# Kernel optimization log

Hardware: AMD Instinct MI355X
Metric: run time of the kernel (lower is better)

Reference implementation:

```python
import jax, jax.numpy as jnp
import numpy as np

B, S, D, H = 2, 2048, 2048, 16
HD = D // H  # 128


def setup_inputs() -> dict:
    key = jax.random.key(0)
    ks = jax.random.split(key, 5)
    scale = 0.02
    return {
        "hidden_states": jax.random.normal(ks[0], (B, S, D), dtype=jnp.float32),
        "Wqkv_w": jax.random.normal(ks[1], (3 * D, D), dtype=jnp.float32) * scale,
        "Wqkv_b": jax.random.normal(ks[2], (3 * D,), dtype=jnp.float32) * scale,
        "out_w": jax.random.normal(ks[3], (D, D), dtype=jnp.float32) * scale,
        "out_b": jax.random.normal(ks[4], (D,), dtype=jnp.float32) * scale,
    }


def reference(hidden_states, Wqkv_w, Wqkv_b, out_w, out_b):
    b, s, d = hidden_states.shape
    # QKV projection (torch Linear: x @ W.T + b)
    qkv = hidden_states @ Wqkv_w.T + Wqkv_b          # [b, s, 3d]
    qkv = qkv.reshape(b, s, 3, H, HD)                 # 'b s (three h d)'
    q, k, v = qkv[:, :, 0], qkv[:, :, 1], qkv[:, :, 2]  # [b, s, h, hd]
    softmax_scale = 1.0 / np.float32(np.sqrt(HD))
    # full quadratic scores, matching the naive baddbmm path
    scores = jnp.einsum('bthd,bshd->bhts', q, k) * softmax_scale  # [b,h,t,s]
    # causal=False (module default), dropout_p=0.0 -> no mask, no dropout
    attn = jax.nn.softmax(scores, axis=-1)
    ctx = jnp.einsum('bhts,bshd->bthd', attn, v)      # [b, t, h, hd]
    ctx = ctx.reshape(b, s, d)
    return ctx @ out_w.T + out_b
```

## Files before the change

### kernel.cpp

```cpp
#include <hip/hip_runtime.h>
#include <cstdint>
#include <cstddef>

#define B_ 2
#define S_ 2048
#define D_ 2048
#define H_ 16
#define HD_ 128
#define NTOK 4096
#define NQKV 6144

typedef unsigned short u16;
typedef __attribute__((ext_vector_type(8))) __bf16 bf16x8;
typedef __attribute__((ext_vector_type(4))) float f32x4;

__device__ __forceinline__ u16 f2bf(float f) {
  uint32_t u = __builtin_bit_cast(uint32_t, f);
  u = (u + 0x7FFFu + ((u >> 16) & 1u)) >> 16;
  return (u16)u;
}

__device__ __forceinline__ void gload_lds16(const void* g, void* l) {
  __builtin_amdgcn_global_load_lds(
      (const __attribute__((address_space(1))) void*)g,
      (__attribute__((address_space(3))) void*)l, 16, 0, 0);
}

__global__ void cvt_all(const float* __restrict__ hs, const float* __restrict__ wqkv,
                        const float* __restrict__ wo,
                        u16* __restrict__ hsb, u16* __restrict__ wqkvb,
                        u16* __restrict__ wob) {
  const int n1 = (B_ * S_ * D_) / 8;
  const int n2 = n1 + (NQKV * D_) / 8;
  const int n3 = n2 + (D_ * D_) / 8;
  int idx = blockIdx.x * blockDim.x + threadIdx.x;
  int stride = gridDim.x * blockDim.x;
  for (int i = idx; i < n3; i += stride) {
    const float* src; u16* dst; int j;
    if (i < n1)      { src = hs;   dst = hsb;   j = i; }
    else if (i < n2) { src = wqkv; dst = wqkvb; j = i - n1; }
    else             { src = wo;   dst = wob;   j = i - n2; }
    const float4* s = (const float4*)(src + (size_t)j * 8);
    float4 a = s[0], b = s[1];
    union { u16 u[8]; uint4 v; } o;
    o.u[0] = f2bf(a.x); o.u[1] = f2bf(a.y); o.u[2] = f2bf(a.z); o.u[3] = f2bf(a.w);
    o.u[4] = f2bf(b.x); o.u[5] = f2bf(b.y); o.u[6] = f2bf(b.z); o.u[7] = f2bf(b.w);
    *(uint4*)(dst + (size_t)j * 8) = o.v;
  }
}

#define PH_MID() do { asm volatile("s_barrier" ::: "memory"); \
  __builtin_amdgcn_s_setprio(1); } while (0)
#define PH_END() do { __builtin_amdgcn_s_setprio(0); \
  asm volatile("s_barrier" ::: "memory"); } while (0)
#define PH_END_VM(n) do { __builtin_amdgcn_s_setprio(0); \
  asm volatile("s_waitcnt vmcnt(" #n ")" ::: "memory"); \
  asm volatile("s_barrier" ::: "memory"); } while (0)


#define STA(sl,buf,ko) gload_lds16(aSrc + (size_t)(sl)*64*D_ + (ko), aDst + (buf)*8192  + (sl)*4096)
#define STB(sl,buf,ko) gload_lds16(bSrc + (size_t)(sl)*64*D_ + (ko), bDst + (buf)*12288 + (sl)*4096)

#define LOADB(buf) do { _Pragma("unroll") for (int nf = 0; nf < 3; ++nf) \
  _Pragma("unroll") for (int kk = 0; kk < 2; ++kk) \
    breg[nf][kk] = *(const bf16x8*)(sB + (buf)*12288 + (wn*48 + nf*16 + fr)*64 + ((((kk<<2)|fq)^swz)<<3)); } while (0)
#define LOADA_A(buf,q) do { _Pragma("unroll") for (int mm = 0; mm < 2; ++mm) \
  _Pragma("unroll") for (int kk = 0; kk < 2; ++kk) \
    arA[mm][kk] = *(const bf16x8*)(sA + (buf)*8192 + (wm*64 + ((q)*2+mm)*16 + fr)*64 + ((((kk<<2)|fq)^swz)<<3)); } while (0)
#define LOADA_B(buf,q) do { _Pragma("unroll") for (int mm = 0; mm < 2; ++mm) \
  _Pragma("unroll") for (int kk = 0; kk < 2; ++kk) \
    arB[mm][kk] = *(const bf16x8*)(sA + (buf)*8192 + (wm*64 + ((q)*2+mm)*16 + fr)*64 + ((((kk<<2)|fq)^swz)<<3)); } while (0)
#define MFMA12_A(q) do { _Pragma("unroll") for (int kk = 0; kk < 2; ++kk) \
  _Pragma("unroll") for (int mm = 0; mm < 2; ++mm) \
  _Pragma("unroll") for (int nf = 0; nf < 3; ++nf) \
    acc[(q)*2+mm][nf] = __builtin_amdgcn_mfma_f32_16x16x32_bf16(arA[mm][kk], breg[nf][kk], acc[(q)*2+mm][nf], 0, 0, 0); } while (0)
#define MFMA12_B(q) do { _Pragma("unroll") for (int kk = 0; kk < 2; ++kk) \
  _Pragma("unroll") for (int mm = 0; mm < 2; ++mm) \
  _Pragma("unroll") for (int nf = 0; nf < 3; ++nf) \
    acc[(q)*2+mm][nf] = __builtin_amdgcn_mfma_f32_16x16x32_bf16(arB[mm][kk], breg[nf][kk], acc[(q)*2+mm][nf], 0, 0, 0); } while (0)

__global__ __launch_bounds__(512, 4) void qkv_gemm(
    const u16* __restrict__ hsb, const u16* __restrict__ wb,
    const float* __restrict__ bias,
    u16* __restrict__ qb, u16* __restrict__ kb, u16* __restrict__ vT)
{
  __shared__ alignas(1024) u16 sA[2 * 8192];
  __shared__ alignas(1024) u16 sB[2 * 12288];
  const int tid = threadIdx.x;
  const int lane = tid & 63, wid = tid >> 6;
  const int wm = wid >> 2, wn = wid & 3;
  const int fr = lane & 15, fq = lane >> 4;
  const int swz = fr & 7;
  const int m0 = blockIdx.x * 128, n0 = blockIdx.y * 192;

  const int r8 = tid >> 3, g8 = (tid & 7) ^ (r8 & 7);
  const u16* aSrc = hsb + (size_t)(m0 + r8) * D_ + g8 * 8;
  const u16* bSrc = wb  + (size_t)(n0 + r8) * D_ + g8 * 8;
  u16* aDst = sA + wid * 512;
  u16* bDst = sB + wid * 512;

  f32x4 acc[4][3];
  f32x4 z = {0.f, 0.f, 0.f, 0.f};
#pragma unroll
  for (int m = 0; m < 4; ++m)
#pragma unroll
    for (int n = 0; n < 3; ++n) acc[m][n] = z;

  bf16x8 breg[3][2], arA[2][2], arB[2][2];

  STB(0,0,0); STB(1,0,0); STB(2,0,0); STA(0,0,0); STA(1,0,0);
  STB(0,1,64); STB(1,1,64); STB(2,1,64);
  asm volatile("s_waitcnt vmcnt(3)" ::: "memory");
  asm volatile("s_barrier" ::: "memory");

#pragma unroll 1
  for (int j = 0; j < 15; ++j) {
    const int kA1 = (2*j + 1) * 64;
    const int kB2 = (2*j + 2) * 64;
    const int kB3 = (2*j + 3) * 64;
    LOADB(0); LOADA_A(0,0); LOADA_B(0,1); STA(0,1,kA1); STA(1,1,kA1);
      PH_MID(); MFMA12_A(0); PH_END();
    STB(0,0,kB2); STB(1,0,kB2); STB(2,0,kB2);
      PH_MID(); MFMA12_B(1); PH_END_VM(3);
    LOADB(1); LOADA_A(1,0); LOADA_B(1,1); STA(0,0,kB2); STA(1,0,kB2);
      PH_MID(); MFMA12_A(0); PH_END();
    STB(0,1,kB3); STB(1,1,kB3); STB(2,1,kB3);
      PH_MID(); MFMA12_B(1); PH_END_VM(3);
  }
  {
    const int kA31 = 31 * 64;
    LOADB(0); LOADA_A(0,0); LOADA_B(0,1); STA(0,1,kA31); STA(1,1,kA31);
      PH_MID(); MFMA12_A(0); PH_END();
      PH_MID(); MFMA12_B(1); PH_END_VM(0);
    LOADB(1); LOADA_A(1,0); LOADA_B(1,1);
      PH_MID(); MFMA12_A(0); PH_END();
      PH_MID(); MFMA12_B(1); PH_END();
  }

  const float qscale = 0.08838834764831845f;
#pragma unroll
  for (int mf = 0; mf < 4; ++mf)
#pragma unroll
    for (int nf = 0; nf < 3; ++nf) {
      int col = n0 + wn * 48 + nf * 16 + fr;
      float bv = bias[col];
      int t = col >> 11;
      int d2 = col & 2047;
      int h = d2 >> 7, hd = d2 & 127;
#pragma unroll
      for (int r = 0; r < 4; ++r) {
        int row = m0 + wm * 64 + mf * 16 + fq * 4 + r;
        int bb = row >> 11, s = row & 2047;
        int bh = bb * H_ + h;
        float val = acc[mf][nf][r] + bv;
        if (t == 0)      qb[((size_t)bh * S_ + s) * HD_ + hd] = f2bf(val * qscale);
        else if (t == 1) kb[((size_t)bh * S_ + s) * HD_ + hd] = f2bf(val);
        else             vT[((size_t)bh * HD_ + hd) * S_ + s] = f2bf(val);
      }
    }
}

#define OSTA(sl,buf,ko) gload_lds16(aSrcO + (size_t)(sl)*64*D_ + (ko), aDstO + (buf)*8192 + (sl)*4096)
#define OSTB(sl,buf,ko) gload_lds16(bSrcO + (size_t)(sl)*64*D_ + (ko), bDstO + (buf)*8192 + (sl)*4096)

#define OLOADB(buf) do { _Pragma("unroll") for (int nf = 0; nf < 2; ++nf) \
  _Pragma("unroll") for (int kk = 0; kk < 2; ++kk) \
    obreg[nf][kk] = *(const bf16x8*)(sB + (buf)*8192 + (wn*32 + nf*16 + fr)*64 + ((((kk<<2)|fq)^swz)<<3)); } while (0)
#define OLOADA_A(buf,q) do { _Pragma("unroll") for (int mm = 0; mm < 2; ++mm) \
  _Pragma("unroll") for (int kk = 0; kk < 2; ++kk) \
    oarA[mm][kk] = *(const bf16x8*)(sA + (buf)*8192 + (wm*64 + ((q)*2+mm)*16 + fr)*64 + ((((kk<<2)|fq)^swz)<<3)); } while (0)
#define OLOADA_B(buf,q) do { _Pragma("unroll") for (int mm = 0; mm < 2; ++mm) \
  _Pragma("unroll") for (int kk = 0; kk < 2; ++kk) \
    oarB[mm][kk] = *(const bf16x8*)(sA + (buf)*8192 + (wm*64 + ((q)*2+mm)*16 + fr)*64 + ((((kk<<2)|fq)^swz)<<3)); } while (0)
#define OMFMA8_A(q) do { _Pragma("unroll") for (int kk = 0; kk < 2; ++kk) \
  _Pragma("unroll") for (int mm = 0; mm < 2; ++mm) \
  _Pragma("unroll") for (int nf = 0; nf < 2; ++nf) \
    acc[(q)*2+mm][nf] = __builtin_amdgcn_mfma_f32_16x16x32_bf16(oarA[mm][kk], obreg[nf][kk], acc[(q)*2+mm][nf], 0, 0, 0); } while (0)
#define OMFMA8_B(q) do { _Pragma("unroll") for (int kk = 0; kk < 2; ++kk) \
  _Pragma("unroll") for (int mm = 0; mm < 2; ++mm) \
  _Pragma("unroll") for (int nf = 0; nf < 2; ++nf) \
    acc[(q)*2+mm][nf] = __builtin_amdgcn_mfma_f32_16x16x32_bf16(oarB[mm][kk], obreg[nf][kk], acc[(q)*2+mm][nf], 0, 0, 0); } while (0)

__global__ __launch_bounds__(512, 4) void out_gemm(
    const u16* __restrict__ ctx, const u16* __restrict__ wo,
    const float* __restrict__ bias, float* __restrict__ out)
{
  __shared__ alignas(1024) u16 sA[2 * 8192];
  __shared__ alignas(1024) u16 sB[2 * 8192];
  const int tid = threadIdx.x;
  const int lane = tid & 63, wid = tid >> 6;
  const int wm = wid >> 2, wn = wid & 3;
  const int fr = lane & 15, fq = lane >> 4;
  const int swz = fr & 7;
  const int m0 = blockIdx.x * 128, n0 = blockIdx.y * 128;

  const int r8 = tid >> 3, g8 = (tid & 7) ^ (r8 & 7);
  const u16* aSrcO = ctx + (size_t)(m0 + r8) * D_ + g8 * 8;
  const u16* bSrcO = wo  + (size_t)(n0 + r8) * D_ + g8 * 8;
  u16* aDstO = sA + wid * 512;
  u16* bDstO = sB + wid * 512;

  f32x4 acc[4][2];
  f32x4 z = {0.f, 0.f, 0.f, 0.f};
#pragma unroll
  for (int m = 0; m < 4; ++m)
#pragma unroll
    for (int n = 0; n < 2; ++n) acc[m][n] = z;

  bf16x8 obreg[2][2], oarA[2][2], oarB[2][2];

  OSTB(0,0,0); OSTB(1,0,0); OSTA(0,0,0); OSTA(1,0,0);
  OSTB(0,1,64); OSTB(1,1,64);
  asm volatile("s_waitcnt vmcnt(2)" ::: "memory");
  asm volatile("s_barrier" ::: "memory");

#pragma unroll 1
  for (int j = 0; j < 15; ++j) {
    const int kA1 = (2*j + 1) * 64;
    const int kB2 = (2*j + 2) * 64;
    const int kB3 = (2*j + 3) * 64;
    OLOADB(0); OLOADA_A(0,0); OLOADA_B(0,1); OSTA(0,1,kA1); OSTA(1,1,kA1);
      PH_MID(); OMFMA8_A(0); PH_END();
    OSTB(0,0,kB2); OSTB(1,0,kB2);
      PH_MID(); OMFMA8_B(1); PH_END_VM(2);
    OLOADB(1); OLOADA_A(1,0); OLOADA_B(1,1); OSTA(0,0,kB2); OSTA(1,0,kB2);
      PH_MID(); OMFMA8_A(0); PH_END();
    OSTB(0,1,kB3); OSTB(1,1,kB3);
      PH_MID(); OMFMA8_B(1); PH_END_VM(2);
  }
  {
    const int kA31 = 31 * 64;
    OLOADB(0); OLOADA_A(0,0); OLOADA_B(0,1); OSTA(0,1,kA31); OSTA(1,1,kA31);
      PH_MID(); OMFMA8_A(0); PH_END();
      PH_MID(); OMFMA8_B(1); PH_END_VM(0);
    OLOADB(1); OLOADA_A(1,0); OLOADA_B(1,1);
      PH_MID(); OMFMA8_A(0); PH_END();
      PH_MID(); OMFMA8_B(1); PH_END();
  }

#pragma unroll
  for (int mf = 0; mf < 4; ++mf)
#pragma unroll
    for (int nf = 0; nf < 2; ++nf) {
      int col = n0 + wn * 32 + nf * 16 + fr;
      float bv = bias[col];
#pragma unroll
      for (int r = 0; r < 4; ++r) {
        int row = m0 + wm * 64 + mf * 16 + fq * 4 + r;
        out[(size_t)row * D_ + col] = acc[mf][nf][r] + bv;
      }
    }
}

#define STAGEKV(kvv, buf) do { _Pragma("unroll") \
  for (int i = 0; i < 4; ++i) { \
    int lk = i * 256 + tid; int rk = lk >> 4, sk = lk & 15; \
    gload_lds16(Kg + (size_t)((kvv) + rk) * HD_ + ((sk ^ (rk & 7)) << 3), \
                &Kl[buf][i * 2048 + wid * 512]); \
    int rv = lk >> 3, sv = lk & 7; \
    gload_lds16(Vg + (size_t)rv * S_ + (kvv) + ((sv ^ (rv & 7)) << 3), \
                &Vl[buf][i * 2048 + wid * 512]); \
  } } while (0)

__global__ __launch_bounds__(256, 2) void attn(
    const u16* __restrict__ qb, const u16* __restrict__ kb,
    const u16* __restrict__ vT, u16* __restrict__ ctx)
{
  __shared__ alignas(1024) u16 Kl[2][64 * 128];
  __shared__ alignas(1024) u16 Vl[2][128 * 64];
  __shared__ alignas(16) u16 Pl[4][32 * 64];

  const int tid = threadIdx.x, lane = tid & 63, wid = tid >> 6;
  const int fr = lane & 15, fq = lane >> 4;
  const int bh = blockIdx.y;
  const int q0 = blockIdx.x * 128 + wid * 32;
  f32x4 z = {0.f, 0.f, 0.f, 0.f};

  const u16* Kg = kb + (size_t)bh * S_ * HD_;
  const u16* Vg = vT + (size_t)bh * HD_ * S_;

  STAGEKV(0, 0);

  const u16* qbase = qb + ((size_t)bh * S_ + q0) * HD_;
  bf16x8 qa[2][4];
#pragma unroll
  for (int h = 0; h < 2; ++h)
#pragma unroll
    for (int kc = 0; kc < 4; ++kc)
      qa[h][kc] = *(const bf16x8*)(qbase + (size_t)(h * 16 + fr) * HD_ + kc * 32 + fq * 8);

  f32x4 accv[2][8];
#pragma unroll
  for (int h = 0; h < 2; ++h)
#pragma unroll
    for (int n = 0; n < 8; ++n) accv[h][n] = z;
  float m_run[2] = {-1e30f, -1e30f};
  float l_run[2] = {0.f, 0.f};

  __syncthreads();
  int cur = 0;

  for (int kv = 0; kv < S_; kv += 64) {
    if (kv + 64 < S_) STAGEKV(kv + 64, cur ^ 1);

    const u16* Kc = Kl[cur];
    const u16* Vc = Vl[cur];

    f32x4 sc[2][4];
    __builtin_amdgcn_s_setprio(1);
#pragma unroll
    for (int j = 0; j < 4; ++j) {
      f32x4 s0 = z, s1 = z;
#pragma unroll
      for (int kc = 0; kc < 4; ++kc) {
        int row = j * 16 + fr;
        bf16x8 kf = *(const bf16x8*)&Kc[row * 128 + ((kc * 32 + fq * 8) ^ ((row & 7) << 3))];
        s0 = __builtin_amdgcn_mfma_f32_16x16x32_bf16(kf, qa[0][kc], s0, 0, 0, 0);
        s1 = __builtin_amdgcn_mfma_f32_16x16x32_bf16(kf, qa[1][kc], s1, 0, 0, 0);
      }
      sc[0][j] = s0; sc[1][j] = s1;
    }
    __builtin_amdgcn_s_setprio(0);

    float pmax[2];
#pragma unroll
    for (int h = 0; h < 2; ++h) {
      float mx = sc[h][0][0];
#pragma unroll
      for (int j = 0; j < 4; ++j)
#pragma unroll
        for (int r = 0; r < 4; ++r) mx = fmaxf(mx, sc[h][j][r]);
      mx = fmaxf(mx, __shfl_xor(mx, 16));
      mx = fmaxf(mx, __shfl_xor(mx, 32));
      pmax[h] = mx;
    }

    int need = (pmax[0] > m_run[0] + 8.f) || (pmax[1] > m_run[1] + 8.f);
    if (__any(need)) {
#pragma unroll
      for (int h = 0; h < 2; ++h) {
        float mn = fmaxf(m_run[h], pmax[h]);
        float corr = __expf(m_run[h] - mn);
        m_run[h] = mn;
        l_run[h] *= corr;
#pragma unroll
        for (int r = 0; r < 4; ++r) {
          float rc = __shfl(corr, (lane & 48) | (fq * 4 + r));
#pragma unroll
          for (int n = 0; n < 8; ++n) accv[h][n][r] *= rc;
        }
      }
    }

    u16* Pw = Pl[wid];
#pragma unroll
    for (int h = 0; h < 2; ++h) {
      float ls = 0.f;
#pragma unroll
      for (int j = 0; j < 4; ++j) {
        union { u16 u[4]; ushort4 v; } pk;
#pragma unroll
        for (int r = 0; r < 4; ++r) {
          float p = __expf(sc[h][j][r] - m_run[h]);
          ls += p;
          pk.u[r] = f2bf(p);
        }
        int prow = h * 16 + fr;
        *(ushort4*)&Pw[prow * 64 + ((j * 16 + fq * 4) ^ ((fr & 7) << 3))] = pk.v;
      }
      ls += __shfl_xor(ls, 16);
      ls += __shfl_xor(ls, 32);
      l_run[h] += ls;
    }

    __builtin_amdgcn_s_setprio(1);
#pragma unroll
    for (int kc = 0; kc < 2; ++kc) {
      int pcol = (kc * 32 + fq * 8) ^ ((fr & 7) << 3);
      bf16x8 pa0 = *(const bf16x8*)&Pw[fr * 64 + pcol];
      bf16x8 pa1 = *(const bf16x8*)&Pw[(16 + fr) * 64 + pcol];
#pragma unroll
      for (int n = 0; n < 8; ++n) {
        int row = n * 16 + fr;
        bf16x8 vf = *(const bf16x8*)&Vc[row * 64 + ((kc * 32 + fq * 8) ^ ((row & 7) << 3))];
        accv[0][n] = __builtin_amdgcn_mfma_f32_16x16x32_bf16(pa0, vf, accv[0][n], 0, 0, 0);
        accv[1][n] = __builtin_amdgcn_mfma_f32_16x16x32_bf16(pa1, vf, accv[1][n], 0, 0, 0);
      }
    }
    __builtin_amdgcn_s_setprio(0);

    __syncthreads();
    cur ^= 1;
  }

  float inv[2][4];
#pragma unroll
  for (int h = 0; h < 2; ++h)
#pragma unroll
    for (int r = 0; r < 4; ++r) {
      float l = __shfl(l_run[h], (lane & 48) | (fq * 4 + r));
      inv[h][r] = 1.f / l;
    }
  u16* cb = ctx + (((size_t)(bh >> 4)) * S_ + q0) * D_ + (size_t)(bh & 15) * HD_;
#pragma unroll
  for (int h = 0; h < 2; ++h)
#pragma unroll
    for (int n = 0; n < 8; ++n)
#pragma unroll
      for (int r = 0; r < 4; ++r) {
        int q = h * 16 + fq * 4 + r;
        cb[(size_t)q * D_ + n * 16 + fr] = f2bf(accv[h][n][r] * inv[h][r]);
      }
}

extern "C" void kernel_launch(void* const* d_in, const int* in_sizes, int n_in,
                              void* d_out, int out_size, void* d_ws, size_t ws_size,
                              hipStream_t stream) {
  const float* hs   = (const float*)d_in[0];
  const float* wqkv = (const float*)d_in[1];
  const float* bqkv = (const float*)d_in[2];
  const float* wo   = (const float*)d_in[3];
  const float* bo   = (const float*)d_in[4];
  float* out = (float*)d_out;

  char* ws = (char*)d_ws;
  u16* hsb   = (u16*)(ws);
  u16* wqkvb = (u16*)(ws + 16777216);
  u16* wob   = (u16*)(ws + 41943040);
  u16* qb    = (u16*)(ws + 50331648);
  u16* kb    = (u16*)(ws + 67108864);
  u16* vT    = (u16*)(ws + 83886080);
  u16* ctx   = (u16*)(ws + 100663296);

  cvt_all<<<2048, 256, 0, stream>>>(hs, wqkv, wo, hsb, wqkvb, wob);

  qkv_gemm<<<dim3(NTOK / 128, NQKV / 192), 512, 0, stream>>>(hsb, wqkvb, bqkv, qb, kb, vT);
  attn<<<dim3(S_ / 128, B_ * H_), 256, 0, stream>>>(qb, kb, vT, ctx);
  out_gemm<<<dim3(NTOK / 128, D_ / 128), 512, 0, stream>>>(ctx, wob, bo, out);
}
```

Measured before the change: 285.7 us.

## Load QKV weight tiles directly from global into registers, bypassing LDS

The QKV GEMM stops staging the weight (B) operand through shared memory. Each wave now prefetches its B fragments straight from global memory into double-buffered registers one k-step ahead, while A is still staged through LDS. This removes the B LDS traffic and halves shared memory per block, which may raise occupancy. The cost is uncoalesced-ish 16-byte global loads per lane, duplicated across the two wm waves, and higher register pressure from the two B fragment sets.

Result: slower. 398.5 us (+39.5%).

```diff
diff --git a/kernel.cpp b/kernel.cpp
--- a/kernel.cpp
+++ b/kernel.cpp
@@ -58,26 +58,18 @@
   asm volatile("s_barrier" ::: "memory"); } while (0)
 
 
-#define STA(sl,buf,ko) gload_lds16(aSrc + (size_t)(sl)*64*D_ + (ko), aDst + (buf)*8192  + (sl)*4096)
-#define STB(sl,buf,ko) gload_lds16(bSrc + (size_t)(sl)*64*D_ + (ko), bDst + (buf)*12288 + (sl)*4096)
-
-#define LOADB(buf) do { _Pragma("unroll") for (int nf = 0; nf < 3; ++nf) \
+#define STA(sl,buf,ko) gload_lds16(aSrc + (size_t)(sl)*64*D_ + (ko), aDst + (buf)*8192 + (sl)*4096)
+
+#define LDA(buf,q) do { _Pragma("unroll") for (int mm = 0; mm < 2; ++mm) \
   _Pragma("unroll") for (int kk = 0; kk < 2; ++kk) \
-    breg[nf][kk] = *(const bf16x8*)(sB + (buf)*12288 + (wn*48 + nf*16 + fr)*64 + ((((kk<<2)|fq)^swz)<<3)); } while (0)
-#define LOADA_A(buf,q) do { _Pragma("unroll") for (int mm = 0; mm < 2; ++mm) \
+    ar[mm][kk] = *(const bf16x8*)(sA + (buf)*8192 + (wm*64 + ((q)*2+mm)*16 + fr)*64 + ((((kk<<2)|fq)^swz)<<3)); } while (0)
+#define PREFB(bg, ko) do { _Pragma("unroll") for (int nf = 0; nf < 3; ++nf) \
   _Pragma("unroll") for (int kk = 0; kk < 2; ++kk) \
-    arA[mm][kk] = *(const bf16x8*)(sA + (buf)*8192 + (wm*64 + ((q)*2+mm)*16 + fr)*64 + ((((kk<<2)|fq)^swz)<<3)); } while (0)
-#define LOADA_B(buf,q) do { _Pragma("unroll") for (int mm = 0; mm < 2; ++mm) \
-  _Pragma("unroll") for (int kk = 0; kk < 2; ++kk) \
-    arB[mm][kk] = *(const bf16x8*)(sA + (buf)*8192 + (wm*64 + ((q)*2+mm)*16 + fr)*64 + ((((kk<<2)|fq)^swz)<<3)); } while (0)
-#define MFMA12_A(q) do { _Pragma("unroll") for (int kk = 0; kk < 2; ++kk) \
+    bg[nf][kk] = *(const bf16x8*)(bBase + (size_t)nf * 16 * D_ + (ko) + kk * 32); } while (0)
+#define MFMA12G(bg, base) do { _Pragma("unroll") for (int kk = 0; kk < 2; ++kk) \
   _Pragma("unroll") for (int mm = 0; mm < 2; ++mm) \
   _Pragma("unroll") for (int nf = 0; nf < 3; ++nf) \
-    acc[(q)*2+mm][nf] = __builtin_amdgcn_mfma_f32_16x16x32_bf16(arA[mm][kk], breg[nf][kk], acc[(q)*2+mm][nf], 0, 0, 0); } while (0)
-#define MFMA12_B(q) do { _Pragma("unroll") for (int kk = 0; kk < 2; ++kk) \
-  _Pragma("unroll") for (int mm = 0; mm < 2; ++mm) \
-  _Pragma("unroll") for (int nf = 0; nf < 3; ++nf) \
-    acc[(q)*2+mm][nf] = __builtin_amdgcn_mfma_f32_16x16x32_bf16(arB[mm][kk], breg[nf][kk], acc[(q)*2+mm][nf], 0, 0, 0); } while (0)
+    acc[(base)+mm][nf] = __builtin_amdgcn_mfma_f32_16x16x32_bf16(ar[mm][kk], bg[nf][kk], acc[(base)+mm][nf], 0, 0, 0); } while (0)
 
 __global__ __launch_bounds__(512, 4) void qkv_gemm(
     const u16* __restrict__ hsb, const u16* __restrict__ wb,
@@ -85,7 +77,6 @@
     u16* __restrict__ qb, u16* __restrict__ kb, u16* __restrict__ vT)
 {
   __shared__ alignas(1024) u16 sA[2 * 8192];
-  __shared__ alignas(1024) u16 sB[2 * 12288];
   const int tid = threadIdx.x;
   const int lane = tid & 63, wid = tid >> 6;
   const int wm = wid >> 2, wn = wid & 3;
@@ -95,9 +86,8 @@
 
   const int r8 = tid >> 3, g8 = (tid & 7) ^ (r8 & 7);
   const u16* aSrc = hsb + (size_t)(m0 + r8) * D_ + g8 * 8;
-  const u16* bSrc = wb  + (size_t)(n0 + r8) * D_ + g8 * 8;
   u16* aDst = sA + wid * 512;
-  u16* bDst = sB + wid * 512;
+  const u16* bBase = wb + (size_t)(n0 + wn * 48 + fr) * D_ + fq * 8;
 
   f32x4 acc[4][3];
   f32x4 z = {0.f, 0.f, 0.f, 0.f};
@@ -106,35 +96,37 @@
 #pragma unroll
     for (int n = 0; n < 3; ++n) acc[m][n] = z;
 
-  bf16x8 breg[3][2], arA[2][2], arB[2][2];
-
-  STB(0,0,0); STB(1,0,0); STB(2,0,0); STA(0,0,0); STA(1,0,0);
-  STB(0,1,64); STB(1,1,64); STB(2,1,64);
-  asm volatile("s_waitcnt vmcnt(3)" ::: "memory");
+  bf16x8 ar[2][2];
+  bf16x8 bgA[3][2], bgB[3][2];
+
+  STA(0,0,0); STA(1,0,0);
+  PREFB(bgA, 0);
+  asm volatile("s_waitcnt vmcnt(6)" ::: "memory");
   asm volatile("s_barrier" ::: "memory");
 
 #pragma unroll 1
   for (int j = 0; j < 15; ++j) {
-    const int kA1 = (2*j + 1) * 64;
-    const int kB2 = (2*j + 2) * 64;
-    const int kB3 = (2*j + 3) * 64;
-    LOADB(0); LOADA_A(0,0); LOADA_B(0,1); STA(0,1,kA1); STA(1,1,kA1);
-      PH_MID(); MFMA12_A(0); PH_END();
-    STB(0,0,kB2); STB(1,0,kB2); STB(2,0,kB2);
-      PH_MID(); MFMA12_B(1); PH_END_VM(3);
-    LOADB(1); LOADA_A(1,0); LOADA_B(1,1); STA(0,0,kB2); STA(1,0,kB2);
-      PH_MID(); MFMA12_A(0); PH_END();
-    STB(0,1,kB3); STB(1,1,kB3); STB(2,1,kB3);
-      PH_MID(); MFMA12_B(1); PH_END_VM(3);
+    const int kN1 = (2*j + 1) * 64;
+    const int kN2 = (2*j + 2) * 64;
+    LDA(0,0); STA(0,1,kN1); STA(1,1,kN1); PREFB(bgB, kN1);
+      PH_MID(); MFMA12G(bgA, 0); PH_END();
+    LDA(0,1);
+      PH_MID(); MFMA12G(bgA, 2); PH_END_VM(6);
+    LDA(1,0); STA(0,0,kN2); STA(1,0,kN2); PREFB(bgA, kN2);
+      PH_MID(); MFMA12G(bgB, 0); PH_END();
+    LDA(1,1);
+      PH_MID(); MFMA12G(bgB, 2); PH_END_VM(6);
   }
   {
-    const int kA31 = 31 * 64;
-    LOADB(0); LOADA_A(0,0); LOADA_B(0,1); STA(0,1,kA31); STA(1,1,kA31);
-      PH_MID(); MFMA12_A(0); PH_END();
-      PH_MID(); MFMA12_B(1); PH_END_VM(0);
-    LOADB(1); LOADA_A(1,0); LOADA_B(1,1);
-      PH_MID(); MFMA12_A(0); PH_END();
-      PH_MID(); MFMA12_B(1); PH_END();
+    const int k31 = 31 * 64;
+    LDA(0,0); STA(0,1,k31); STA(1,1,k31); PREFB(bgB, k31);
+      PH_MID(); MFMA12G(bgA, 0); PH_END();
+    LDA(0,1);
+      PH_MID(); MFMA12G(bgA, 2); PH_END_VM(6);
+    LDA(1,0);
+      PH_MID(); MFMA12G(bgB, 0); PH_END();
+    LDA(1,1);
+      PH_MID(); MFMA12G(bgB, 2); PH_END();
   }
 
   const float qscale = 0.08838834764831845f;
```
